# Performance work log

Hardware: AMD Instinct MI355X
Metric: run time of the kernel (lower is better)

## Reference

```python
import jax, jax.numpy as jnp
import numpy as np

K = 1.0  # Lorentz curvature
N, H, IN_S, OUT_S = 4096, 12, 256, 128  # nodes, heads, spatial in/out dims


def _midpoint_norm(ave):
    # Lorentz midpoint normalization: sqrt(K) * ave / sqrt(|<ave,ave>_L|)
    inner = -ave[..., 0:1] ** 2 + jnp.sum(ave[..., 1:] ** 2, axis=-1, keepdims=True)
    denom = jnp.sqrt(jnp.maximum(jnp.abs(inner), 1e-8))
    return jnp.sqrt(K) * ave / denom


def setup_inputs() -> dict:
    key = jax.random.key(0)
    ks = jax.random.split(key, 8)
    xs = jax.random.normal(ks[0], (N, IN_S), jnp.float32)
    xt = jnp.sqrt(jnp.sum(xs * xs, axis=-1, keepdims=True) + K)
    x_lorentz = jnp.concatenate([xt, xs], axis=-1)  # [N, 257] on the manifold
    std = 1.0 / np.sqrt(IN_S)
    def lin(k1, k2):
        W = jax.random.uniform(k1, (H, OUT_S, IN_S), jnp.float32, -std, std)
        b = jax.random.uniform(k2, (H, OUT_S), jnp.float32, -std, std)
        return W, b
    Wq, bq = lin(ks[1], ks[2])
    Wk, bk = lin(ks[3], ks[4])
    Wv, bv = lin(ks[5], ks[6])
    scale = jnp.array([np.sqrt(OUT_S + 1)], jnp.float32)  # sqrt(out_channels)
    bias = jnp.zeros((), jnp.float32)
    return {"x_lorentz": x_lorentz, "Wq": Wq, "bq": bq, "Wk": Wk, "bk": bk,
            "Wv": Wv, "bv": bv, "scale": scale, "bias": bias}


def reference(x_lorentz, Wq, bq, Wk, bk, Wv, bv, scale, bias):
    xs = x_lorentz[..., 1:]  # drop time coord: [N, IN_S]

    def hyp_linear(W, b):
        # per-head linear on spatial part, then reconstruct Lorentz time coord
        s = jnp.einsum('ni,hoi->hno', xs, W) + b[:, None, :]  # [H, N, OUT_S]
        t = jnp.sqrt(jnp.sum(s * s, axis=-1, keepdims=True) + K)
        return jnp.concatenate([t, s], axis=-1)  # [H, N, OUT_S+1]

    q = hyp_linear(Wq, bq)
    k = hyp_linear(Wk, bk)
    v = hyp_linear(Wv, bv)

    # Lorentz inner product scores: <q,k>_L = -q0*k0 + q_s . k_s
    sgn = jnp.concatenate([-jnp.ones((1,), q.dtype), jnp.ones((q.shape[-1] - 1,), q.dtype)])
    att = 2.0 + 2.0 * jnp.einsum('hnd,hmd->hnm', q * sgn, k)  # [H, N, N]
    att = att / scale + bias
    att = jax.nn.softmax(att, axis=-1)

    # weighted Lorentz midpoint per head
    ave = jnp.einsum('hnm,hmd->hnd', att, v)
    out = _midpoint_norm(ave)           # [H, N, D]
    out = out.transpose(1, 0, 2)        # [N, H, D]
    # uniform midpoint across heads
    out = _midpoint_norm(out.mean(axis=-2))  # [N, D]
    return out
```

## Files before the change

### kernel.cpp

```cpp
#include <hip/hip_runtime.h>
#include <hip/hip_bf16.h>

#define NT   4096
#define NH   12
#define INS  256
#define DOUT 128
#define D1   129
#define PSTR 132

typedef __attribute__((ext_vector_type(8))) short bf16x8;
typedef __attribute__((ext_vector_type(4))) float f32x4;

__device__ __forceinline__ short f2bf(float f) {
  union { __hip_bfloat16 h; short s; } u;
  u.h = __float2bfloat16(f);
  return u.s;
}
__device__ __forceinline__ float bf2f(short s) {
  union { unsigned u; float f; } v;
  v.u = ((unsigned)(unsigned short)s) << 16;
  return v.f;
}

#define MFMA16(a,b,c) __builtin_amdgcn_mfma_f32_16x16x32_bf16((a),(b),(c),0,0,0)

#define GL2LDS(gp, lp) \
  __builtin_amdgcn_global_load_lds((const __attribute__((address_space(1))) unsigned*)(gp), \
                                   (__attribute__((address_space(3))) unsigned*)(lp), 16, 0, 0)


__global__ void k_cvt_xs(const float* __restrict__ xl, short* __restrict__ xs) {
  int i = blockIdx.x * 256 + threadIdx.x;
  int row = i >> 8, col = i & 255;
  xs[i] = f2bf(xl[row * 257 + 1 + col]);
}

__global__ void k_cvt_w(const float* __restrict__ w0, const float* __restrict__ w1,
                        const float* __restrict__ w2, short* __restrict__ dst) {
  int i = blockIdx.x * 256 + threadIdx.x;
  const float* s = blockIdx.y == 0 ? w0 : (blockIdx.y == 1 ? w1 : w2);
  dst[(size_t)blockIdx.y * (NH * DOUT * INS) + i] = f2bf(s[i]);
}


__launch_bounds__(256, 2)
__global__ void k_proj(const short* __restrict__ xs, const short* __restrict__ Wb,
                       const float* __restrict__ b0, const float* __restrict__ b1,
                       const float* __restrict__ b2, const float* __restrict__ scalep,
                       short* __restrict__ Qb, short* __restrict__ Kb, short* __restrict__ VT,
                       float* __restrict__ qt, float* __restrict__ kt, float* __restrict__ vt) {
  __shared__ __align__(16) short vlds[128][144];
  int t = threadIdx.x, l = t & 63, w = t >> 6;
  int lr = l & 15, lg = l >> 4;
  int h = blockIdx.y, z = blockIdx.z;
  int n0w = blockIdx.x * 128 + w * 32;
  const short* Wh = Wb + ((size_t)z * NH + h) * DOUT * INS;
  const float* bias = z == 0 ? b0 : (z == 1 ? b1 : b2);

  f32x4 acc[2][8] = {};
#pragma unroll
  for (int dk = 0; dk < 8; ++dk) {
    bf16x8 a[2], b[8];
#pragma unroll
    for (int qf = 0; qf < 2; ++qf)
      a[qf] = *(const bf16x8*)(xs + (size_t)(n0w + 16 * qf + lr) * INS + dk * 32 + lg * 8);
#pragma unroll
    for (int cf = 0; cf < 8; ++cf)
      b[cf] = *(const bf16x8*)(Wh + (size_t)(lr + 16 * cf) * INS + dk * 32 + lg * 8);
#pragma unroll
    for (int qf = 0; qf < 2; ++qf)
#pragma unroll
      for (int cf = 0; cf < 8; ++cf)
        acc[qf][cf] = MFMA16(a[qf], b[cf], acc[qf][cf]);
  }

  float tval[2][4];
#pragma unroll
  for (int qf = 0; qf < 2; ++qf) {
    float ssq[4] = {0.f, 0.f, 0.f, 0.f};
#pragma unroll
    for (int cf = 0; cf < 8; ++cf) {
      float bv = bias[h * DOUT + lr + 16 * cf];
#pragma unroll
      for (int r = 0; r < 4; ++r) {
        acc[qf][cf][r] += bv;
        ssq[r] += acc[qf][cf][r] * acc[qf][cf][r];
      }
    }
#pragma unroll
    for (int r = 0; r < 4; ++r) {
      float s = ssq[r];
      s += __shfl_xor(s, 1); s += __shfl_xor(s, 2);
      s += __shfl_xor(s, 4); s += __shfl_xor(s, 8);
      tval[qf][r] = sqrtf(s + 1.0f);
    }
  }

  if (z < 2) {
    float f = (z == 0) ? (2.0f * 1.442695040888963f / scalep[0]) : 1.0f;
    short* Ob = (z == 0) ? Qb : Kb;
    float* Ot = (z == 0) ? qt : kt;
#pragma unroll
    for (int qf = 0; qf < 2; ++qf)
#pragma unroll
      for (int r = 0; r < 4; ++r) {
        int n = n0w + 16 * qf + lg * 4 + r;
#pragma unroll
        for (int cf = 0; cf < 8; ++cf)
          Ob[((size_t)h * NT + n) * DOUT + lr + 16 * cf] = f2bf(acc[qf][cf][r] * f);
        if (lr == 0) Ot[(size_t)h * NT + n] = tval[qf][r] * f;
      }
  } else {
#pragma unroll
    for (int qf = 0; qf < 2; ++qf)
#pragma unroll
      for (int cf = 0; cf < 8; ++cf)
#pragma unroll
        for (int r = 0; r < 4; ++r) {
          int nl = w * 32 + 16 * qf + lg * 4 + r;
          vlds[lr + 16 * cf][nl] = f2bf(acc[qf][cf][r]);
        }
#pragma unroll
    for (int qf = 0; qf < 2; ++qf)
#pragma unroll
      for (int r = 0; r < 4; ++r) {
        int n = n0w + 16 * qf + lg * 4 + r;
        if (lr == 0) vt[(size_t)h * NT + n] = tval[qf][r];
      }
    __syncthreads();
    int d = t >> 1, half = t & 1;
    const short* src = &vlds[d][half * 64];
    short* dst = VT + ((size_t)h * DOUT + d) * NT + blockIdx.x * 128 + half * 64;
#pragma unroll
    for (int j = 0; j < 8; ++j)
      *(bf16x8*)(dst + j * 8) = *(const bf16x8*)(src + j * 8);
  }
}


#define PROWB 144
#define PWAVE (32 * PROWB)

__launch_bounds__(256, 2)
__global__ void k_attn(const short* __restrict__ Qb, const short* __restrict__ Kb,
                       const short* __restrict__ VT,
                       const float* __restrict__ qt, const float* __restrict__ ktp,
                       const float* __restrict__ vtp, float* __restrict__ part) {
  __shared__ __align__(16) char lds_k[64 * 256];
  __shared__ __align__(16) char lds_v[128 * 128];
  __shared__ __align__(16) char lds_p[4 * PWAVE];

  int t = threadIdx.x, l = t & 63, w = t >> 6;
  int lr = l & 15, lg = l >> 4;
  int h = blockIdx.y, z = blockIdx.z;
  int n0w = blockIdx.x * 128 + w * 32;

  const short* Qh = Qb + (size_t)h * NT * DOUT;
  const short* Kh = Kb + (size_t)h * NT * DOUT;
  const short* VTh = VT + (size_t)h * DOUT * NT;
  const float* qth = qt + (size_t)h * NT;
  const float* kth = ktp + (size_t)h * NT;
  const float* vth = vtp + (size_t)h * NT;

  bf16x8 aq[2][4];
#pragma unroll
  for (int qf = 0; qf < 2; ++qf)
#pragma unroll
    for (int dk = 0; dk < 4; ++dk)
      aq[qf][dk] = *(const bf16x8*)(Qh + (size_t)(n0w + 16 * qf + lr) * DOUT + dk * 32 + lg * 8);
  float qc2[2][4];
#pragma unroll
  for (int qf = 0; qf < 2; ++qf)
#pragma unroll
    for (int r = 0; r < 4; ++r)
      qc2[qf][r] = qth[n0w + 16 * qf + lg * 4 + r];

  f32x4 accO[2][8] = {};
  float avt_run[2][4] = {};

  int kc_m = t >> 2, kc_s = (t & 3);
  (void)kc_m; (void)kc_s;

  {
    int m0 = z * (NT / 2);
#pragma unroll
    for (int it = 0; it < 4; ++it) {
      int c = t + it * 256;
      int m = c >> 4, s = c & 15;
      GL2LDS(Kh + (size_t)(m0 + m) * DOUT + ((s ^ (m & 7)) * 8), lds_k + c * 16);
    }
  }

  for (int ktile = 0; ktile < NT / 128; ++ktile) {
    int m0 = z * (NT / 2) + ktile * 64;
    __syncthreads();

#pragma unroll
    for (int it = 0; it < 4; ++it) {
      int c = t + it * 256;
      int d = c >> 3, s = c & 7;
      GL2LDS(VTh + (size_t)d * NT + m0 + ((s ^ (d & 7)) * 8), lds_v + c * 16);
    }
    float ktv[4], vtv[4];
#pragma unroll
    for (int mf = 0; mf < 4; ++mf) {
      ktv[mf] = kth[m0 + lr + 16 * mf];
      vtv[mf] = vth[m0 + lr + 16 * mf];
    }

    f32x4 accS[2][4] = {};
#pragma unroll
    for (int dk = 0; dk < 4; ++dk) {
      bf16x8 bk[4];
#pragma unroll
      for (int mf = 0; mf < 4; ++mf) {
        int m = lr + 16 * mf;
        int slot = (4 * dk + lg) ^ (m & 7);
        bk[mf] = *(const bf16x8*)(lds_k + m * 256 + slot * 16);
      }
#pragma unroll
      for (int qf = 0; qf < 2; ++qf)
#pragma unroll
        for (int mf = 0; mf < 4; ++mf)
          accS[qf][mf] = MFMA16(aq[qf][dk], bk[mf], accS[qf][mf]);
    }

#pragma unroll
    for (int qf = 0; qf < 2; ++qf) {
#pragma unroll
      for (int r = 0; r < 4; ++r) {
        int ql = lg * 4 + r + 16 * qf;
        short* prow = (short*)(lds_p + w * PWAVE + ql * PROWB);
        float pv = 0.f;
#pragma unroll
        for (int mf = 0; mf < 4; ++mf) {
          float a2 = fmaf(-qc2[qf][r], ktv[mf], accS[qf][mf][r]);
          float p;
          asm("v_exp_f32 %0, %1" : "=v"(p) : "v"(a2));
          short pb = f2bf(p);
          prow[lr + 16 * mf] = pb;
          pv = fmaf(bf2f(pb), vtv[mf], pv);
        }
        avt_run[qf][r] += pv;
      }
    }

    __syncthreads();

    if (ktile + 1 < NT / 128) {
      int m1 = m0 + 64;
#pragma unroll
      for (int it = 0; it < 4; ++it) {
        int c = t + it * 256;
        int m = c >> 4, s = c & 15;
        GL2LDS(Kh + (size_t)(m1 + m) * DOUT + ((s ^ (m & 7)) * 8), lds_k + c * 16);
      }
    }

#pragma unroll
    for (int ks = 0; ks < 2; ++ks) {
      bf16x8 ap[2];
#pragma unroll
      for (int qf = 0; qf < 2; ++qf)
        ap[qf] = *(const bf16x8*)(lds_p + w * PWAVE + (16 * qf + lr) * PROWB + ks * 64 + lg * 16);
      bf16x8 bv[8];
#pragma unroll
      for (int df = 0; df < 8; ++df) {
        int d = lr + 16 * df;
        int slot = (4 * ks + lg) ^ (d & 7);
        bv[df] = *(const bf16x8*)(lds_v + d * 128 + slot * 16);
      }
#pragma unroll
      for (int qf = 0; qf < 2; ++qf)
#pragma unroll
        for (int df = 0; df < 8; ++df)
          accO[qf][df] = MFMA16(ap[qf], bv[df], accO[qf][df]);
    }
  }

#pragma unroll
  for (int qf = 0; qf < 2; ++qf)
#pragma unroll
    for (int r = 0; r < 4; ++r) {
      float av = avt_run[qf][r];
      av += __shfl_xor(av, 1); av += __shfl_xor(av, 2);
      av += __shfl_xor(av, 4); av += __shfl_xor(av, 8);
      int n = n0w + 16 * qf + lg * 4 + r;
      float* base = part + ((size_t)h * NT + n) * PSTR;
#pragma unroll
      for (int df = 0; df < 8; ++df)
        atomicAdd(base + lr + 16 * df, accO[qf][df][r]);
      if (lr == 0) atomicAdd(base + 128, av);
    }
}


__global__ void k_comb(const float* __restrict__ part, float* __restrict__ out) {
  int l = threadIdx.x & 63, w = threadIdx.x >> 6;
  int n = blockIdx.x * 4 + w;
  float acc_lo = 0.f, acc_hi = 0.f, acc_t = 0.f;
#pragma unroll
  for (int h = 0; h < NH; ++h) {
    const float* p = part + ((size_t)h * NT + n) * PSTR;
    float x = p[l], y = p[64 + l], at = p[128];
    float sp = x * x + y * y;
    sp += __shfl_xor(sp, 1);  sp += __shfl_xor(sp, 2);
    sp += __shfl_xor(sp, 4);  sp += __shfl_xor(sp, 8);
    sp += __shfl_xor(sp, 16); sp += __shfl_xor(sp, 32);
    float inner = sp - at * at;
    float rd = 1.0f / sqrtf(fmaxf(fabsf(inner), 1e-8f));
    acc_lo += x * rd; acc_hi += y * rd; acc_t += at * rd;
  }
  float sp = acc_lo * acc_lo + acc_hi * acc_hi;
  sp += __shfl_xor(sp, 1);  sp += __shfl_xor(sp, 2);
  sp += __shfl_xor(sp, 4);  sp += __shfl_xor(sp, 8);
  sp += __shfl_xor(sp, 16); sp += __shfl_xor(sp, 32);
  float inner = sp - acc_t * acc_t;
  float rd = 1.0f / sqrtf(fmaxf(fabsf(inner), 1e-8f));
  float* orow = out + (size_t)n * D1;
  orow[1 + l] = acc_lo * rd;
  orow[65 + l] = acc_hi * rd;
  if (l == 0) orow[0] = acc_t * rd;
}


extern "C" void kernel_launch(void* const* d_in, const int* in_sizes, int n_in,
                              void* d_out, int out_size, void* d_ws, size_t ws_size,
                              hipStream_t stream) {
  (void)in_sizes; (void)n_in; (void)out_size; (void)ws_size;
  const float* xl    = (const float*)d_in[0];
  const float* Wq    = (const float*)d_in[1];
  const float* bq    = (const float*)d_in[2];
  const float* Wk    = (const float*)d_in[3];
  const float* bk    = (const float*)d_in[4];
  const float* Wv    = (const float*)d_in[5];
  const float* bv    = (const float*)d_in[6];
  const float* scale = (const float*)d_in[7];
  float* out = (float*)d_out;

  char* ws = (char*)d_ws;
  size_t off = 0;
  auto alloc = [&](size_t b) { char* p = ws + off; off = (off + b + 255) & ~(size_t)255; return p; };
  short* xs    = (short*)alloc((size_t)NT * INS * 2);
  short* Wb    = (short*)alloc((size_t)3 * NH * DOUT * INS * 2);
  short* Qb    = (short*)alloc((size_t)NH * NT * DOUT * 2);
  short* Kb    = (short*)alloc((size_t)NH * NT * DOUT * 2);
  short* VT    = (short*)alloc((size_t)NH * DOUT * NT * 2);
  float* qt    = (float*)alloc((size_t)NH * NT * 4);
  float* kt    = (float*)alloc((size_t)NH * NT * 4);
  float* vt    = (float*)alloc((size_t)NH * NT * 4);
  float* part  = (float*)alloc((size_t)NH * NT * PSTR * 4);

  hipMemsetAsync(part, 0, (size_t)NH * NT * PSTR * 4, stream);
  k_cvt_xs<<<NT, 256, 0, stream>>>(xl, xs);
  k_cvt_w<<<dim3(NH * DOUT * INS / 256, 3), 256, 0, stream>>>(Wq, Wk, Wv, Wb);
  k_proj<<<dim3(NT / 128, NH, 3), 256, 0, stream>>>(xs, Wb, bq, bk, bv, scale, Qb, Kb, VT, qt, kt, vt);
  k_attn<<<dim3(NT / 128, NH, 2), 256, 0, stream>>>(Qb, Kb, VT, qt, kt, vt, part);
  k_comb<<<NT / 4, 256, 0, stream>>>(part, out);
}
```

Measured before the change: 323.2 us.

## Switch attention to 32x32 MFMA with register-resident P via permlane swaps

The attention kernel moves from 16x16x32 to 32x32x16 bf16 MFMA and computes S transposed (K as A operand, Q as B), so each lane holds the scores of one query. The exp'd probabilities are packed to bf16 and rearranged with v_permlane32_swap into the B-operand fragment for the PV MFMA, which removes the per-wave LDS P buffer and its stores and loads. K and V time coordinates are written by the projection kernel in a permuted order so they can be read as float4 vectors matching the MFMA output layout. The projection kernel now stages Q and K through LDS for coalesced row stores, and the attention occupancy hint rises to 3 blocks. The risks are the correctness of the permutation and swap logic, and higher register pressure from the larger accumulators.

```diff
diff --git a/kernel.cpp b/kernel.cpp
--- a/kernel.cpp
+++ b/kernel.cpp
@@ -8,21 +8,18 @@
 #define D1   129
 #define PSTR 132
 
-typedef __attribute__((ext_vector_type(8))) short bf16x8;
-typedef __attribute__((ext_vector_type(4))) float f32x4;
+typedef short bf16x8  __attribute__((ext_vector_type(8)));
+typedef float f32x4   __attribute__((ext_vector_type(4)));
+typedef float f32x16  __attribute__((ext_vector_type(16)));
 
 __device__ __forceinline__ short f2bf(float f) {
   union { __hip_bfloat16 h; short s; } u;
   u.h = __float2bfloat16(f);
   return u.s;
 }
-__device__ __forceinline__ float bf2f(short s) {
-  union { unsigned u; float f; } v;
-  v.u = ((unsigned)(unsigned short)s) << 16;
-  return v.f;
-}
 
 #define MFMA16(a,b,c) __builtin_amdgcn_mfma_f32_16x16x32_bf16((a),(b),(c),0,0,0)
+#define MFMA32(a,b,c) __builtin_amdgcn_mfma_f32_32x32x16_bf16((a),(b),(c),0,0,0)
 
 #define GL2LDS(gp, lp) \
   __builtin_amdgcn_global_load_lds((const __attribute__((address_space(1))) unsigned*)(gp), \
@@ -48,8 +45,8 @@
                        const float* __restrict__ b0, const float* __restrict__ b1,
                        const float* __restrict__ b2, const float* __restrict__ scalep,
                        short* __restrict__ Qb, short* __restrict__ Kb, short* __restrict__ VT,
-                       float* __restrict__ qt, float* __restrict__ kt, float* __restrict__ vt) {
-  __shared__ __align__(16) short vlds[128][144];
+                       float* __restrict__ qt, float* __restrict__ ktP, float* __restrict__ vtP) {
+  __shared__ __align__(16) short lds_t[128 * 144];
   int t = threadIdx.x, l = t & 63, w = t >> 6;
   int lr = l & 15, lg = l >> 4;
   int h = blockIdx.y, z = blockIdx.z;
@@ -96,40 +93,61 @@
     }
   }
 
+  float c2 = 2.0f * 1.442695040888963f / scalep[0];
+
   if (z < 2) {
-    float f = (z == 0) ? (2.0f * 1.442695040888963f / scalep[0]) : 1.0f;
-    short* Ob = (z == 0) ? Qb : Kb;
-    float* Ot = (z == 0) ? qt : kt;
+    float f = (z == 0) ? c2 : 1.0f;
 #pragma unroll
     for (int qf = 0; qf < 2; ++qf)
 #pragma unroll
-      for (int r = 0; r < 4; ++r) {
-        int n = n0w + 16 * qf + lg * 4 + r;
-#pragma unroll
-        for (int cf = 0; cf < 8; ++cf)
-          Ob[((size_t)h * NT + n) * DOUT + lr + 16 * cf] = f2bf(acc[qf][cf][r] * f);
-        if (lr == 0) Ot[(size_t)h * NT + n] = tval[qf][r] * f;
-      }
+      for (int cf = 0; cf < 8; ++cf)
+#pragma unroll
+        for (int r = 0; r < 4; ++r)
+          lds_t[(w * 32 + 16 * qf + lg * 4 + r) * 136 + lr + 16 * cf] = f2bf(acc[qf][cf][r] * f);
+    if (lr == 0) {
+#pragma unroll
+      for (int qf = 0; qf < 2; ++qf)
+#pragma unroll
+        for (int r = 0; r < 4; ++r) {
+          int n = n0w + 16 * qf + lg * 4 + r;
+          if (z == 0) {
+            qt[(size_t)h * NT + n] = tval[qf][r] * f;
+          } else {
+            int ml = n & 31, g = n >> 5;
+            int hh = (ml >> 2) & 1, j = (ml & 3) + 4 * (ml >> 3);
+            ktP[(size_t)h * NT + g * 32 + hh * 16 + j] = tval[qf][r];
+          }
+        }
+    }
+    __syncthreads();
+    int row = t >> 1, half = t & 1;
+    const short* src = lds_t + row * 136 + half * 64;
+    short* dst = (z == 0 ? Qb : Kb) + ((size_t)h * NT + blockIdx.x * 128 + row) * DOUT + half * 64;
+#pragma unroll
+    for (int j = 0; j < 8; ++j)
+      *(bf16x8*)(dst + j * 8) = *(const bf16x8*)(src + j * 8);
   } else {
 #pragma unroll
     for (int qf = 0; qf < 2; ++qf)
 #pragma unroll
       for (int cf = 0; cf < 8; ++cf)
 #pragma unroll
+        for (int r = 0; r < 4; ++r)
+          lds_t[(lr + 16 * cf) * 144 + w * 32 + 16 * qf + lg * 4 + r] = f2bf(acc[qf][cf][r]);
+    if (lr == 0) {
+#pragma unroll
+      for (int qf = 0; qf < 2; ++qf)
+#pragma unroll
         for (int r = 0; r < 4; ++r) {
-          int nl = w * 32 + 16 * qf + lg * 4 + r;
-          vlds[lr + 16 * cf][nl] = f2bf(acc[qf][cf][r]);
+          int n = n0w + 16 * qf + lg * 4 + r;
+          int ml = n & 31, g = n >> 5;
+          int hh = (ml >> 2) & 1, j = (ml & 3) + 4 * (ml >> 3);
+          vtP[(size_t)h * NT + g * 32 + hh * 16 + j] = tval[qf][r];
         }
-#pragma unroll
-    for (int qf = 0; qf < 2; ++qf)
-#pragma unroll
-      for (int r = 0; r < 4; ++r) {
-        int n = n0w + 16 * qf + lg * 4 + r;
-        if (lr == 0) vt[(size_t)h * NT + n] = tval[qf][r];
-      }
+    }
     __syncthreads();
     int d = t >> 1, half = t & 1;
-    const short* src = &vlds[d][half * 64];
+    const short* src = lds_t + d * 144 + half * 64;
     short* dst = VT + ((size_t)h * DOUT + d) * NT + blockIdx.x * 128 + half * 64;
 #pragma unroll
     for (int j = 0; j < 8; ++j)
@@ -138,48 +156,34 @@
 }
 
 
-#define PROWB 144
-#define PWAVE (32 * PROWB)
-
-__launch_bounds__(256, 2)
+__launch_bounds__(256, 3)
 __global__ void k_attn(const short* __restrict__ Qb, const short* __restrict__ Kb,
                        const short* __restrict__ VT,
-                       const float* __restrict__ qt, const float* __restrict__ ktp,
-                       const float* __restrict__ vtp, float* __restrict__ part) {
+                       const float* __restrict__ qt, const float* __restrict__ ktP,
+                       const float* __restrict__ vtP, float* __restrict__ part) {
   __shared__ __align__(16) char lds_k[64 * 256];
   __shared__ __align__(16) char lds_v[128 * 128];
-  __shared__ __align__(16) char lds_p[4 * PWAVE];
 
   int t = threadIdx.x, l = t & 63, w = t >> 6;
-  int lr = l & 15, lg = l >> 4;
+  int ql = l & 31, hi = l >> 5;
   int h = blockIdx.y, z = blockIdx.z;
   int n0w = blockIdx.x * 128 + w * 32;
+  int n = n0w + ql;
 
   const short* Qh = Qb + (size_t)h * NT * DOUT;
   const short* Kh = Kb + (size_t)h * NT * DOUT;
   const short* VTh = VT + (size_t)h * DOUT * NT;
-  const float* qth = qt + (size_t)h * NT;
-  const float* kth = ktp + (size_t)h * NT;
-  const float* vth = vtp + (size_t)h * NT;
-
-  bf16x8 aq[2][4];
-#pragma unroll
-  for (int qf = 0; qf < 2; ++qf)
-#pragma unroll
-    for (int dk = 0; dk < 4; ++dk)
-      aq[qf][dk] = *(const bf16x8*)(Qh + (size_t)(n0w + 16 * qf + lr) * DOUT + dk * 32 + lg * 8);
-  float qc2[2][4];
-#pragma unroll
-  for (int qf = 0; qf < 2; ++qf)
-#pragma unroll
-    for (int r = 0; r < 4; ++r)
-      qc2[qf][r] = qth[n0w + 16 * qf + lg * 4 + r];
-
-  f32x4 accO[2][8] = {};
-  float avt_run[2][4] = {};
-
-  int kc_m = t >> 2, kc_s = (t & 3);
-  (void)kc_m; (void)kc_s;
+  const float* ktPh = ktP + (size_t)h * NT;
+  const float* vtPh = vtP + (size_t)h * NT;
+
+  bf16x8 bq[8];
+#pragma unroll
+  for (int dk = 0; dk < 8; ++dk)
+    bq[dk] = *(const bf16x8*)(Qh + (size_t)n * DOUT + dk * 16 + hi * 8);
+  float qc2 = qt[(size_t)h * NT + n];
+
+  f32x16 accO[4] = {};
+  float avt = 0.f;
 
   {
     int m0 = z * (NT / 2);
@@ -187,7 +191,7 @@
     for (int it = 0; it < 4; ++it) {
       int c = t + it * 256;
       int m = c >> 4, s = c & 15;
-      GL2LDS(Kh + (size_t)(m0 + m) * DOUT + ((s ^ (m & 7)) * 8), lds_k + c * 16);
+      GL2LDS(Kh + (size_t)(m0 + m) * DOUT + ((s ^ (m & 15)) * 8), lds_k + c * 16);
     }
   }
 
@@ -201,48 +205,50 @@
       int d = c >> 3, s = c & 7;
       GL2LDS(VTh + (size_t)d * NT + m0 + ((s ^ (d & 7)) * 8), lds_v + c * 16);
     }
-    float ktv[4], vtv[4];
-#pragma unroll
-    for (int mf = 0; mf < 4; ++mf) {
-      ktv[mf] = kth[m0 + lr + 16 * mf];
-      vtv[mf] = vth[m0 + lr + 16 * mf];
-    }
-
-    f32x4 accS[2][4] = {};
-#pragma unroll
-    for (int dk = 0; dk < 4; ++dk) {
-      bf16x8 bk[4];
-#pragma unroll
-      for (int mf = 0; mf < 4; ++mf) {
-        int m = lr + 16 * mf;
-        int slot = (4 * dk + lg) ^ (m & 7);
-        bk[mf] = *(const bf16x8*)(lds_k + m * 256 + slot * 16);
-      }
-#pragma unroll
-      for (int qf = 0; qf < 2; ++qf)
-#pragma unroll
-        for (int mf = 0; mf < 4; ++mf)
-          accS[qf][mf] = MFMA16(aq[qf][dk], bk[mf], accS[qf][mf]);
-    }
-
-#pragma unroll
-    for (int qf = 0; qf < 2; ++qf) {
-#pragma unroll
-      for (int r = 0; r < 4; ++r) {
-        int ql = lg * 4 + r + 16 * qf;
-        short* prow = (short*)(lds_p + w * PWAVE + ql * PROWB);
-        float pv = 0.f;
-#pragma unroll
-        for (int mf = 0; mf < 4; ++mf) {
-          float a2 = fmaf(-qc2[qf][r], ktv[mf], accS[qf][mf][r]);
-          float p;
-          asm("v_exp_f32 %0, %1" : "=v"(p) : "v"(a2));
-          short pb = f2bf(p);
-          prow[lr + 16 * mf] = pb;
-          pv = fmaf(bf2f(pb), vtv[mf], pv);
+
+    bf16x8 pfrag[4];
+#pragma unroll
+    for (int mf = 0; mf < 2; ++mf) {
+      f32x16 accS = {};
+      int m = mf * 32 + ql;
+      int rowb = m * 256;
+      int sx = m & 15;
+#pragma unroll
+      for (int dk = 0; dk < 8; ++dk) {
+        bf16x8 ak = *(const bf16x8*)(lds_k + rowb + (((dk * 2 + hi) ^ sx) * 16));
+        accS = MFMA32(ak, bq[dk], accS);
+      }
+
+      const float* ktm = ktPh + m0 + mf * 32 + hi * 16;
+      const float* vtm = vtPh + m0 + mf * 32 + hi * 16;
+      unsigned pk[8];
+#pragma unroll
+      for (int i4 = 0; i4 < 4; ++i4) {
+        f32x4 kt4 = *(const f32x4*)(ktm + i4 * 4);
+        f32x4 vt4 = *(const f32x4*)(vtm + i4 * 4);
+#pragma unroll
+        for (int ii = 0; ii < 2; ++ii) {
+          float a0 = fmaf(-qc2, kt4[2 * ii],     accS[i4 * 4 + 2 * ii]);
+          float a1 = fmaf(-qc2, kt4[2 * ii + 1], accS[i4 * 4 + 2 * ii + 1]);
+          float p0, p1;
+          asm("v_exp_f32 %0, %1" : "=v"(p0) : "v"(a0));
+          asm("v_exp_f32 %0, %1" : "=v"(p1) : "v"(a1));
+          avt = fmaf(p0, vt4[2 * ii], avt);
+          avt = fmaf(p1, vt4[2 * ii + 1], avt);
+          unsigned pw;
+          asm("v_cvt_pk_bf16_f32 %0, %1, %2" : "=v"(pw) : "v"(p0), "v"(p1));
+          pk[i4 * 2 + ii] = pw;
         }
-        avt_run[qf][r] += pv;
-      }
+      }
+      asm volatile("v_permlane32_swap_b32 %0, %1" : "+v"(pk[0]), "+v"(pk[2]));
+      asm volatile("v_permlane32_swap_b32 %0, %1" : "+v"(pk[1]), "+v"(pk[3]));
+      asm volatile("v_permlane32_swap_b32 %0, %1" : "+v"(pk[4]), "+v"(pk[6]));
+      asm volatile("v_permlane32_swap_b32 %0, %1" : "+v"(pk[5]), "+v"(pk[7]));
+      union { unsigned u[4]; bf16x8 v; } f0, f1;
+      f0.u[0] = pk[0]; f0.u[1] = pk[1]; f0.u[2] = pk[2]; f0.u[3] = pk[3];
+      f1.u[0] = pk[4]; f1.u[1] = pk[5]; f1.u[2] = pk[6]; f1.u[3] = pk[7];
+      pfrag[2 * mf] = f0.v;
+      pfrag[2 * mf + 1] = f1.v;
     }
 
     __syncthreads();
@@ -253,45 +259,30 @@
       for (int it = 0; it < 4; ++it) {
         int c = t + it * 256;
         int m = c >> 4, s = c & 15;
-        GL2LDS(Kh + (size_t)(m1 + m) * DOUT + ((s ^ (m & 7)) * 8), lds_k + c * 16);
-      }
-    }
-
-#pragma unroll
-    for (int ks = 0; ks < 2; ++ks) {
-      bf16x8 ap[2];
-#pragma unroll
-      for (int qf = 0; qf < 2; ++qf)
-        ap[qf] = *(const bf16x8*)(lds_p + w * PWAVE + (16 * qf + lr) * PROWB + ks * 64 + lg * 16);
-      bf16x8 bv[8];
-#pragma unroll
-      for (int df = 0; df < 8; ++df) {
-        int d = lr + 16 * df;
-        int slot = (4 * ks + lg) ^ (d & 7);
-        bv[df] = *(const bf16x8*)(lds_v + d * 128 + slot * 16);
-      }
-#pragma unroll
-      for (int qf = 0; qf < 2; ++qf)
-#pragma unroll
-        for (int df = 0; df < 8; ++df)
-          accO[qf][df] = MFMA16(ap[qf], bv[df], accO[qf][df]);
-    }
-  }
-
-#pragma unroll
-  for (int qf = 0; qf < 2; ++qf)
-#pragma unroll
-    for (int r = 0; r < 4; ++r) {
-      float av = avt_run[qf][r];
-      av += __shfl_xor(av, 1); av += __shfl_xor(av, 2);
-      av += __shfl_xor(av, 4); av += __shfl_xor(av, 8);
-      int n = n0w + 16 * qf + lg * 4 + r;
-      float* base = part + ((size_t)h * NT + n) * PSTR;
-#pragma unroll
-      for (int df = 0; df < 8; ++df)
-        atomicAdd(base + lr + 16 * df, accO[qf][df][r]);
-      if (lr == 0) atomicAdd(base + 128, av);
-    }
+        GL2LDS(Kh + (size_t)(m1 + m) * DOUT + ((s ^ (m & 15)) * 8), lds_k + c * 16);
+      }
+    }
+
+#pragma unroll
+    for (int ks = 0; ks < 4; ++ks) {
+#pragma unroll
+      for (int df = 0; df < 4; ++df) {
+        int d = df * 32 + ql;
+        bf16x8 av = *(const bf16x8*)(lds_v + d * 128 + (((ks * 2 + hi) ^ (d & 7)) * 16));
+        accO[df] = MFMA32(av, pfrag[ks], accO[df]);
+      }
+    }
+  }
+
+  float* base = part + ((size_t)h * NT + n) * PSTR;
+#pragma unroll
+  for (int df = 0; df < 4; ++df)
+#pragma unroll
+    for (int r = 0; r < 16; ++r) {
+      int dd = df * 32 + (r & 3) + 8 * (r >> 2) + 4 * hi;
+      atomicAdd(base + dd, accO[df][r]);
+    }
+  atomicAdd(base + 128, avt);
 }
 
 
@@ -347,14 +338,14 @@
   short* Kb    = (short*)alloc((size_t)NH * NT * DOUT * 2);
   short* VT    = (short*)alloc((size_t)NH * DOUT * NT * 2);
   float* qt    = (float*)alloc((size_t)NH * NT * 4);
-  float* kt    = (float*)alloc((size_t)NH * NT * 4);
-  float* vt    = (float*)alloc((size_t)NH * NT * 4);
+  float* ktP   = (float*)alloc((size_t)NH * NT * 4);
+  float* vtP   = (float*)alloc((size_t)NH * NT * 4);
   float* part  = (float*)alloc((size_t)NH * NT * PSTR * 4);
 
   hipMemsetAsync(part, 0, (size_t)NH * NT * PSTR * 4, stream);
   k_cvt_xs<<<NT, 256, 0, stream>>>(xl, xs);
   k_cvt_w<<<dim3(NH * DOUT * INS / 256, 3), 256, 0, stream>>>(Wq, Wk, Wv, Wb);
-  k_proj<<<dim3(NT / 128, NH, 3), 256, 0, stream>>>(xs, Wb, bq, bk, bv, scale, Qb, Kb, VT, qt, kt, vt);
-  k_attn<<<dim3(NT / 128, NH, 2), 256, 0, stream>>>(Qb, Kb, VT, qt, kt, vt, part);
+  k_proj<<<dim3(NT / 128, NH, 3), 256, 0, stream>>>(xs, Wb, bq, bk, bv, scale, Qb, Kb, VT, qt, ktP, vtP);
+  k_attn<<<dim3(NT / 128, NH, 2), 256, 0, stream>>>(Qb, Kb, VT, qt, ktP, vtP, part);
   k_comb<<<NT / 4, 256, 0, stream>>>(part, out);
 }
```

After: 708.9 us. +119.3%, slower.
